# Kernel tuning notes

Measured on AMD Instinct MI355X. Metric: run time of the kernel, lower is better.

The kernel has to match this reference:

```python
import jax, jax.numpy as jnp
import numpy as np

B, S_SRC, L_SRC, S_TGT, L_TGT, C = 4, 8, 512, 8, 512, 4
K_PALETTE = 97
PAD = -1.0
TAU = 0.1
EPS = 1e-15


def setup_inputs() -> dict:
    key = jax.random.key(0)
    k1, k2, k3, k4, k5, k6 = jax.random.split(key, 6)
    palette = jax.random.uniform(k1, (K_PALETTE, C), dtype=jnp.float32)
    src_idx = jax.random.randint(k2, (B, S_SRC, L_SRC), 0, K_PALETTE)
    tgt_idx = jax.random.randint(k3, (B, S_TGT, L_TGT), 0, K_PALETTE)
    src = palette[src_idx]
    tgt = palette[tgt_idx]
    pad_vec = jnp.full((C,), PAD, dtype=jnp.float32)
    src = jnp.where(jax.random.uniform(k4, (B, S_SRC, L_SRC, 1)) < 0.03, pad_vec, src)
    tgt = jnp.where(jax.random.uniform(k5, (B, S_TGT, L_TGT, 1)) < 0.03, pad_vec, tgt)
    seg_sim_map = jax.random.normal(k6, (B, S_TGT * L_TGT, S_SRC * L_SRC), dtype=jnp.float32)
    return {"seg_sim_map": seg_sim_map, "seg_colors_src": src, "seg_colors_tgt": tgt}


def _loss(seg_sim_map, seg_colors_src, seg_colors_tgt):
    Bb = seg_sim_map.shape[0]
    src_flat = seg_colors_src.reshape(Bb, -1, C)   # [B, Nsrc, C]
    tgt_flat = seg_colors_tgt.reshape(Bb, -1, C)   # [B, Ntgt, C]
    valid_src = ~jnp.all(src_flat == PAD, axis=-1)  # [B, Nsrc]
    valid_tgt = ~jnp.all(tgt_flat == PAD, axis=-1)  # [B, Ntgt]

    # eq[b,t,j]: valid tgt row t's color exactly equals valid src column j's color.
    # This replaces torch.unique + index_add: aggregating softmax mass over src
    # positions sharing the gt color is identical to index_add by color index
    # followed by gathering the gt color's bucket.
    eq = jnp.all(tgt_flat[:, :, None, :] == src_flat[:, None, :, :], axis=-1)
    eq = eq & valid_src[:, None, :] & valid_tgt[:, :, None]      # [B, Ntgt, Nsrc]
    matched = jnp.any(eq, axis=-1)                               # rows kept by nll mask

    # masked softmax over valid src columns == softmax over the sliced columns
    logits = jnp.where(valid_src[:, None, :], seg_sim_map / TAU, -jnp.inf)
    probs = jax.nn.softmax(logits, axis=-1)                      # [B, Ntgt, Nsrc]

    p_gt = jnp.einsum('btj,btj->bt', probs, eq.astype(probs.dtype))
    nll = -jnp.log(p_gt + EPS)                                   # [B, Ntgt]

    nll = nll.reshape(Bb, S_TGT, L_TGT)
    m = matched.reshape(Bb, S_TGT, L_TGT).astype(nll.dtype)
    nvalid = m.sum(-1)                                           # [B, S_tgt]
    seg_loss = jnp.where(nvalid > 0, (nll * m).sum(-1) / jnp.maximum(nvalid, 1.0), 0.0)
    cnt = jnp.sum((nvalid > 0).astype(jnp.int32))
    total = seg_loss.sum() / jnp.maximum(cnt, 1).astype(seg_loss.dtype)
    return total, cnt


def reference(seg_sim_map, seg_colors_src, seg_colors_tgt):
    return _loss(seg_sim_map, seg_colors_src, seg_colors_tgt)
```

## Files before the change

kernel.cpp:

```cpp
#include <hip/hip_runtime.h>
#include <math.h>

#define NSRC 4096
#define NTGT 4096
#define NB 4
#define L2SCALE (10.0f * 1.4426950408889634f)
#define PADBITS 0xBF800000u

__device__ __forceinline__ float fexp2(float x) { return __builtin_amdgcn_exp2f(x); }


__device__ __forceinline__ unsigned mix128(uint4 c) {
    unsigned h = c.x * 0x9E3779B1u;
    h ^= h >> 15; h *= 0x85EBCA77u;
    h ^= c.y;     h *= 0xC2B2AE3Du;
    h ^= h >> 13;
    h ^= c.z;     h *= 0x27D4EB2Fu;
    h ^= h >> 16;
    h ^= c.w;     h *= 0x9E3779B1u;
    h ^= h >> 15;
    return h | 1u;
}

__global__ __launch_bounds__(256) void key_kernel(const uint4* __restrict__ srcc,
                                                  const uint4* __restrict__ tgtc,
                                                  unsigned* __restrict__ skey,
                                                  float* __restrict__ sbias,
                                                  unsigned* __restrict__ tkey) {
    int i = blockIdx.x * 256 + threadIdx.x;
    if (i < NB * NSRC) {
        uint4 c = srcc[i];
        bool pad = (c.x == PADBITS) && (c.y == PADBITS) && (c.z == PADBITS) && (c.w == PADBITS);
        skey[i] = pad ? 0u : mix128(c);
        sbias[i] = pad ? -1048576.0f : 0.0f;
    } else {
        int j = i - NB * NSRC;
        uint4 c = tgtc[j];
        bool pad = (c.x == PADBITS) && (c.y == PADBITS) && (c.z == PADBITS) && (c.w == PADBITS);
        tkey[j] = pad ? 2u : mix128(c);
    }
}


__global__ __launch_bounds__(256) void row_kernel(const float* __restrict__ sim,
                                                  const unsigned* __restrict__ skey,
                                                  const float* __restrict__ sbias,
                                                  const unsigned* __restrict__ tkey,
                                                  float* __restrict__ row_out) {
    const int wave = threadIdx.x >> 6;
    const int lane = threadIdx.x & 63;
    const int row = blockIdx.x * 4 + wave;
    const int b = row >> 12;
    const float4* simv = (const float4*)(sim + (size_t)row * NSRC);
    const uint4* keyv = (const uint4*)(skey + (size_t)b * NSRC);
    const float4* biasv = (const float4*)(sbias + (size_t)b * NSRC);
    const unsigned tk = tkey[row];

    float s0 = 0.f, s1 = 0.f, s2 = 0.f, s3 = 0.f;
    float g0 = 0.f, g1 = 0.f, g2 = 0.f, g3 = 0.f;

#define PROC(LV, BV, KV, SA, GA)                                         \
    do {                                                                 \
        float _e = fexp2(fmaf((LV), L2SCALE, (BV)));                     \
        SA += _e;                                                        \
        GA += ((KV) == tk) ? _e : 0.f;                                   \
    } while (0)

    #pragma unroll
    for (int it = 0; it < 16; ++it) {
        int j4 = it * 64 + lane;
        float4 l4 = simv[j4];
        uint4 k4 = keyv[j4];
        float4 b4 = biasv[j4];
        PROC(l4.x, b4.x, k4.x, s0, g0);
        PROC(l4.y, b4.y, k4.y, s1, g1);
        PROC(l4.z, b4.z, k4.z, s2, g2);
        PROC(l4.w, b4.w, k4.w, s3, g3);
    }
#undef PROC

    float sf = (s0 + s1) + (s2 + s3);
    float sg = (g0 + g1) + (g2 + g3);
    #pragma unroll
    for (int off = 1; off < 64; off <<= 1) {
        sf += __shfl_xor(sf, off);
        sg += __shfl_xor(sg, off);
    }

    if (lane == 0) {
        row_out[row] = (sg > 0.f) ? -logf(sg / sf + 1e-15f) : -1.0f;
    }
}


__global__ __launch_bounds__(1024) void finalize_kernel(const float* __restrict__ row_out,
                                                        float* __restrict__ out) {
    __shared__ float ssum[32], scnt[32];
    int wave = threadIdx.x >> 6, lane = threadIdx.x & 63;
    for (int seg = wave; seg < 32; seg += 16) {
        float a = 0.f, c = 0.f;
        for (int j = lane; j < 512; j += 64) {
            float v = row_out[seg * 512 + j];
            bool m = (v > -0.5f);
            a += m ? v : 0.f;
            c += m ? 1.f : 0.f;
        }
        #pragma unroll
        for (int off = 1; off < 64; off <<= 1) {
            a += __shfl_xor(a, off);
            c += __shfl_xor(c, off);
        }
        if (lane == 0) { ssum[seg] = a; scnt[seg] = c; }
    }
    __syncthreads();
    if (threadIdx.x == 0) {
        float tot = 0.f;
        int cnt = 0;
        for (int i = 0; i < 32; ++i) {
            if (scnt[i] > 0.f) { tot += ssum[i] / scnt[i]; cnt++; }
        }
        out[0] = (cnt > 0) ? tot / (float)cnt : 0.f;
        out[1] = (float)cnt;
    }
}


extern "C" void kernel_launch(void* const* d_in, const int* in_sizes, int n_in,
                              void* d_out, int out_size, void* d_ws, size_t ws_size,
                              hipStream_t stream) {
    const float* sim = (const float*)d_in[0];
    const uint4* src = (const uint4*)d_in[1];
    const uint4* tgt = (const uint4*)d_in[2];
    float* out = (float*)d_out;

    unsigned* skey = (unsigned*)d_ws;
    float* sbias = (float*)(skey + NB * NSRC);
    unsigned* tkey = (unsigned*)(sbias + NB * NSRC);
    float* row_out = (float*)(tkey + NB * NTGT);

    key_kernel<<<(NB * (NSRC + NTGT)) / 256, 256, 0, stream>>>(src, tgt, skey, sbias, tkey);
    row_kernel<<<NB * NTGT / 4, 256, 0, stream>>>(sim, skey, sbias, tkey, row_out);
    finalize_kernel<<<1, 1024, 0, stream>>>(row_out, out);
}
```

Baseline: 60.06 us.

## Fuse key hashing into row kernel with LDS-resident source keys

Measured after the change: 58.32 us. 1.03x faster.

```diff
diff --git a/kernel.cpp b/kernel.cpp
--- a/kernel.cpp
+++ b/kernel.cpp
@@ -8,7 +8,6 @@
 #define PADBITS 0xBF800000u
 
 __device__ __forceinline__ float fexp2(float x) { return __builtin_amdgcn_exp2f(x); }
-
 
 __device__ __forceinline__ unsigned mix128(uint4 c) {
     unsigned h = c.x * 0x9E3779B1u;
@@ -22,46 +21,41 @@
     return h | 1u;
 }
 
-__global__ __launch_bounds__(256) void key_kernel(const uint4* __restrict__ srcc,
+
+__global__ __launch_bounds__(512) void row_kernel(const float* __restrict__ sim,
+                                                  const uint4* __restrict__ srcc,
                                                   const uint4* __restrict__ tgtc,
-                                                  unsigned* __restrict__ skey,
-                                                  float* __restrict__ sbias,
-                                                  unsigned* __restrict__ tkey) {
-    int i = blockIdx.x * 256 + threadIdx.x;
-    if (i < NB * NSRC) {
-        uint4 c = srcc[i];
-        bool pad = (c.x == PADBITS) && (c.y == PADBITS) && (c.z == PADBITS) && (c.w == PADBITS);
-        skey[i] = pad ? 0u : mix128(c);
-        sbias[i] = pad ? -1048576.0f : 0.0f;
-    } else {
-        int j = i - NB * NSRC;
-        uint4 c = tgtc[j];
-        bool pad = (c.x == PADBITS) && (c.y == PADBITS) && (c.z == PADBITS) && (c.w == PADBITS);
-        tkey[j] = pad ? 2u : mix128(c);
-    }
-}
-
-
-__global__ __launch_bounds__(256) void row_kernel(const float* __restrict__ sim,
-                                                  const unsigned* __restrict__ skey,
-                                                  const float* __restrict__ sbias,
-                                                  const unsigned* __restrict__ tkey,
                                                   float* __restrict__ row_out) {
+    __shared__ unsigned lkey[NSRC];
     const int wave = threadIdx.x >> 6;
     const int lane = threadIdx.x & 63;
-    const int row = blockIdx.x * 4 + wave;
-    const int b = row >> 12;
+    const int row0 = blockIdx.x * 8;
+    const int b = row0 >> 12;
+
+    #pragma unroll
+    for (int u = 0; u < 8; ++u) {
+        int j = u * 512 + threadIdx.x;
+        uint4 c = srcc[b * NSRC + j];
+        bool pad = (c.x == PADBITS) && (c.y == PADBITS) && (c.z == PADBITS) && (c.w == PADBITS);
+        lkey[j] = pad ? 0u : mix128(c);
+    }
+    __syncthreads();
+
+    const int row = row0 + wave;
+    uint4 tc = tgtc[row];
+    bool tpad = (tc.x == PADBITS) && (tc.y == PADBITS) && (tc.z == PADBITS) && (tc.w == PADBITS);
+    const unsigned tk = tpad ? 2u : mix128(tc);
+
     const float4* simv = (const float4*)(sim + (size_t)row * NSRC);
-    const uint4* keyv = (const uint4*)(skey + (size_t)b * NSRC);
-    const float4* biasv = (const float4*)(sbias + (size_t)b * NSRC);
-    const unsigned tk = tkey[row];
+    const uint4* keyv = (const uint4*)lkey;
 
     float s0 = 0.f, s1 = 0.f, s2 = 0.f, s3 = 0.f;
     float g0 = 0.f, g1 = 0.f, g2 = 0.f, g3 = 0.f;
 
-#define PROC(LV, BV, KV, SA, GA)                                         \
+#define PROC(LV, KV, SA, GA)                                             \
     do {                                                                 \
-        float _e = fexp2(fmaf((LV), L2SCALE, (BV)));                     \
+        float _arg = ((KV) != 0u) ? (LV) * L2SCALE : -1048576.0f;        \
+        float _e = fexp2(_arg);                                          \
         SA += _e;                                                        \
         GA += ((KV) == tk) ? _e : 0.f;                                   \
     } while (0)
@@ -71,11 +65,10 @@
         int j4 = it * 64 + lane;
         float4 l4 = simv[j4];
         uint4 k4 = keyv[j4];
-        float4 b4 = biasv[j4];
-        PROC(l4.x, b4.x, k4.x, s0, g0);
-        PROC(l4.y, b4.y, k4.y, s1, g1);
-        PROC(l4.z, b4.z, k4.z, s2, g2);
-        PROC(l4.w, b4.w, k4.w, s3, g3);
+        PROC(l4.x, k4.x, s0, g0);
+        PROC(l4.y, k4.y, s1, g1);
+        PROC(l4.z, k4.z, s2, g2);
+        PROC(l4.w, k4.w, s3, g3);
     }
 #undef PROC
 
@@ -133,12 +126,8 @@
     const uint4* tgt = (const uint4*)d_in[2];
     float* out = (float*)d_out;
 
-    unsigned* skey = (unsigned*)d_ws;
-    float* sbias = (float*)(skey + NB * NSRC);
-    unsigned* tkey = (unsigned*)(sbias + NB * NSRC);
-    float* row_out = (float*)(tkey + NB * NTGT);
+    float* row_out = (float*)d_ws;
 
-    key_kernel<<<(NB * (NSRC + NTGT)) / 256, 256, 0, stream>>>(src, tgt, skey, sbias, tkey);
-    row_kernel<<<NB * NTGT / 4, 256, 0, stream>>>(sim, skey, sbias, tkey, row_out);
+    row_kernel<<<NB * NTGT / 8, 512, 0, stream>>>(sim, src, tgt, row_out);
     finalize_kernel<<<1, 1024, 0, stream>>>(row_out, out);
 }
```
